# Optimization experiments

Measured on AMD Instinct MI355X. Metric: run time of the kernel, lower is better.

Reference implementation:

```python
import jax, jax.numpy as jnp
import numpy as np

B, K, H, W = 8, 32, 480, 480
N, D = 576, 1024
NUM_CLASSES, CLS_DIM, OUT = 150, 64, 256
IN_DIM = D + CLS_DIM + 5


def setup_inputs() -> dict:
    key = jax.random.key(0)
    ks = jax.random.split(key, 8)
    return {
        "feature_map": jax.random.normal(ks[0], (B, N, D), dtype=jnp.float32),
        "masks": jax.random.randint(ks[1], (B, K, H, W), 0, 2, dtype=jnp.int32),
        "class_ids": jax.random.randint(ks[2], (B, K), 0, NUM_CLASSES, dtype=jnp.int64),
        "embed_table": jax.random.normal(ks[3], (NUM_CLASSES, CLS_DIM), dtype=jnp.float32),
        "W1": jax.random.normal(ks[4], (IN_DIM, OUT), dtype=jnp.float32) * 0.02,
        "b1": jnp.zeros((OUT,), dtype=jnp.float32),
        "ln_g": jnp.ones((OUT,), dtype=jnp.float32),
        "ln_b": jnp.zeros((OUT,), dtype=jnp.float32),
        "W2": jax.random.normal(ks[5], (OUT, OUT), dtype=jnp.float32) * 0.02,
        "b2": jnp.zeros((OUT,), dtype=jnp.float32),
    }


def _geom_feats(m):
    # m: [B,K,H,W] float binary masks -> [B,K,5] (cx, cy, area_norm, bbox_w, bbox_h)
    dt = m.dtype
    area = m.sum((-2, -1))                      # [B,K]
    safe = jnp.maximum(area, 1.0)
    xs = jnp.arange(W, dtype=dt)
    ys = jnp.arange(H, dtype=dt)
    cx = jnp.einsum('bkhw,w->bk', m, xs) / safe / W
    cy = jnp.einsum('bkhw,h->bk', m, ys) / safe / H
    col = m.max(axis=2)                          # [B,K,W] column occupancy
    row = m.max(axis=3)                          # [B,K,H] row occupancy
    x_min = jnp.min(jnp.where(col > 0, xs, float(W)), axis=-1)
    x_max = jnp.max(jnp.where(col > 0, xs, -1.0), axis=-1)
    y_min = jnp.min(jnp.where(row > 0, ys, float(H)), axis=-1)
    y_max = jnp.max(jnp.where(row > 0, ys, -1.0), axis=-1)
    bbox_w = (x_max - x_min + 1.0) / W
    bbox_h = (y_max - y_min + 1.0) / H
    area_norm = area / (H * W)
    geom = jnp.stack([cx, cy, area_norm, bbox_w, bbox_h], axis=-1)  # [B,K,5]
    valid = (area >= 1.0)[..., None]
    return jnp.where(valid, geom, 0.0)


def reference(feature_map, masks, class_ids, embed_table, W1, b1, ln_g, ln_b, W2, b2):
    Hf = Wf = int(round(N ** 0.5))  # 24
    m = (masks > 0).astype(feature_map.dtype)           # [B,K,H,W]
    # nearest-neighbor downsample (PyTorch 'nearest': src = floor(dst*in/out))
    idx_h = (jnp.arange(Hf) * H) // Hf
    idx_w = (jnp.arange(Wf) * W) // Wf
    m_rs = m[:, :, idx_h][:, :, :, idx_w]               # [B,K,Hf,Wf]
    m_flat = m_rs.reshape(B, K, Hf * Wf)                # [B,K,N]
    msum = jnp.clip(m_flat.sum(-1, keepdims=True), 1e-6, None)
    pooled = jnp.einsum('bkn,bnd->bkd', m_flat, feature_map) / msum  # [B,K,D]
    geom = _geom_feats(m)                               # [B,K,5]
    cls_emb = embed_table[class_ids]                    # [B,K,CLS_DIM]
    x = jnp.concatenate([pooled, cls_emb, geom], axis=-1)  # [B,K,IN_DIM]
    h = jax.nn.gelu(x @ W1 + b1, approximate=False)
    mu = h.mean(-1, keepdims=True)
    var = jnp.mean((h - mu) ** 2, axis=-1, keepdims=True)
    hn = (h - mu) * jax.lax.rsqrt(var + 1e-5) * ln_g + ln_b
    return hn @ W2 + b2                                 # [B,K,OUT]
```

## Files before the change

kernel.cpp:

```cpp
#include <hip/hip_runtime.h>
#include <math.h>

#define Bb 8
#define Kk 32
#define Hh 480
#define Ww 480
#define Nn 576
#define Dd 1024
#define CLSD 64
#define OUTD 256
#define INDIM 1093
#define INPAD 1152
#define BK 256
#define PIX4 57600

#define DS_OFF   0
#define META_OFF 147456
#define X_OFF    149504

__global__ __launch_bounds__(1024) void kA(const int* __restrict__ masks,
                                           float* __restrict__ ws) {
  const int bk = blockIdx.x;
  const int t  = threadIdx.x;
  const int4* mp = (const int4*)(masks + (size_t)bk * (Hh * Ww));

  __shared__ float ds[576];
  __shared__ int s_area, s_sumx, s_sumy, s_cnt;
  __shared__ int s_minx, s_maxx, s_miny, s_maxy;
  if (t == 0) {
    s_area = 0; s_sumx = 0; s_sumy = 0; s_cnt = 0;
    s_minx = Ww; s_maxx = -1; s_miny = Hh; s_maxy = -1;
  }
  __syncthreads();

  int area = 0, sumx = 0, sumy = 0, cntds = 0;
  int minx = Ww, maxx = -1, miny = Hh, maxy = -1;

  for (int q = t; q < PIX4; q += 1024) {
    int4 v = mp[q];
    int h   = q / 120;
    int rem = q - h * 120;
    int w0  = rem * 4;
    int m0 = v.x > 0, m1 = v.y > 0, m2 = v.z > 0, m3 = v.w > 0;
    int c = m0 + m1 + m2 + m3;
    area += c;
    sumy += h * c;
    sumx += w0 * c + m1 + 2 * m2 + 3 * m3;
    if (c) {
      miny = min(miny, h);
      maxy = max(maxy, h);
      int lo = m0 ? w0 : (m1 ? w0 + 1 : (m2 ? w0 + 2 : w0 + 3));
      int hi = m3 ? w0 + 3 : (m2 ? w0 + 2 : (m1 ? w0 + 1 : w0));
      minx = min(minx, lo);
      maxx = max(maxx, hi);
    }
    int a20 = h / 20;
    int c5  = rem / 5;
    if (h == a20 * 20 && rem == c5 * 5) {
      ds[a20 * 24 + c5] = (float)m0;
      cntds += m0;
    }
  }

  for (int off = 32; off; off >>= 1) {
    area  += __shfl_down(area, off);
    sumx  += __shfl_down(sumx, off);
    sumy  += __shfl_down(sumy, off);
    cntds += __shfl_down(cntds, off);
    minx = min(minx, __shfl_down(minx, off));
    maxx = max(maxx, __shfl_down(maxx, off));
    miny = min(miny, __shfl_down(miny, off));
    maxy = max(maxy, __shfl_down(maxy, off));
  }
  if ((t & 63) == 0) {
    atomicAdd(&s_area, area);
    atomicAdd(&s_sumx, sumx);
    atomicAdd(&s_sumy, sumy);
    atomicAdd(&s_cnt, cntds);
    atomicMin(&s_minx, minx);
    atomicMax(&s_maxx, maxx);
    atomicMin(&s_miny, miny);
    atomicMax(&s_maxy, maxy);
  }
  __syncthreads();

  float* ws_ds = ws + DS_OFF + (size_t)bk * 576;
  if (t < 576) ws_ds[t] = ds[t];

  if (t == 0) {
    float* meta = ws + META_OFF + (size_t)bk * 8;
    float areaf = (float)s_area;
    float safe  = fmaxf(areaf, 1.0f);
    float cx = ((float)s_sumx / safe) * (1.0f / Ww);
    float cy = ((float)s_sumy / safe) * (1.0f / Hh);
    float an = areaf * (1.0f / (Hh * Ww));
    float bw = (float)(s_maxx - s_minx + 1) * (1.0f / Ww);
    float bh = (float)(s_maxy - s_miny + 1) * (1.0f / Hh);
    if (s_area < 1) { cx = 0.f; cy = 0.f; an = 0.f; bw = 0.f; bh = 0.f; }
    meta[0] = cx; meta[1] = cy; meta[2] = an; meta[3] = bw; meta[4] = bh;
    meta[5] = 1.0f / fmaxf((float)s_cnt, 1e-6f);
    meta[6] = (float)s_cnt;
  }
}

__global__ __launch_bounds__(256) void kB(const float* __restrict__ fm,
                                          const int* __restrict__ cids,
                                          const float* __restrict__ emb,
                                          float* __restrict__ ws) {
  const int b  = blockIdx.x & 7;
  const int k  = blockIdx.x >> 3;
  const int bk = b * Kk + k;
  const int t  = threadIdx.x;

  __shared__ float msh[576];
  __shared__ int act[576];
  __shared__ int nact;
  if (t == 0) nact = 0;
  __syncthreads();

  const float* ws_ds = ws + DS_OFF + (size_t)bk * 576;
  for (int i = t; i < 576; i += 256) {
    float mv = ws_ds[i];
    msh[i] = mv;
    if (mv != 0.0f) {
      int p = atomicAdd(&nact, 1);
      act[p] = i;
    }
  }
  __syncthreads();
  const int na = nact;

  float ax = 0.f, ay = 0.f, az = 0.f, aw = 0.f;
  const float4* fmp = (const float4*)fm + (size_t)b * Nn * (Dd / 4);
  int j = 0;
  for (; j + 4 <= na; j += 4) {
    int4 nn = *(const int4*)(act + j);
    float4 f0 = fmp[nn.x * (Dd / 4) + t];
    float4 f1 = fmp[nn.y * (Dd / 4) + t];
    float4 f2 = fmp[nn.z * (Dd / 4) + t];
    float4 f3 = fmp[nn.w * (Dd / 4) + t];
    ax += f0.x + f1.x + f2.x + f3.x;
    ay += f0.y + f1.y + f2.y + f3.y;
    az += f0.z + f1.z + f2.z + f3.z;
    aw += f0.w + f1.w + f2.w + f3.w;
  }
  for (; j < na; j++) {
    float4 f = fmp[act[j] * (Dd / 4) + t];
    ax += f.x; ay += f.y; az += f.z; aw += f.w;
  }

  const float* meta = ws + META_OFF + (size_t)bk * 8;
  float inv = meta[5];
  float* xrow = ws + X_OFF + (size_t)bk * INPAD;
  float4 p4;
  p4.x = ax * inv; p4.y = ay * inv; p4.z = az * inv; p4.w = aw * inv;
  ((float4*)xrow)[t] = p4;

  if (t < CLSD) {
    int cid = cids[bk];
    xrow[Dd + t] = emb[cid * CLSD + t];
  } else if (t < CLSD + 5) {
    xrow[Dd + CLSD + (t - CLSD)] = meta[t - CLSD];
  } else if (t < CLSD + 5 + (INPAD - INDIM)) {
    xrow[INDIM + (t - CLSD - 5)] = 0.0f;
  }
}

__global__ __launch_bounds__(256) void kC(float* __restrict__ ws,
                                          const float* __restrict__ W1,
                                          const float* __restrict__ b1,
                                          const float* __restrict__ lg,
                                          const float* __restrict__ lb,
                                          const float* __restrict__ W2,
                                          const float* __restrict__ b2,
                                          float* __restrict__ out) {
  const int o  = threadIdx.x;
  const int r0 = blockIdx.x * 2;
  const float* x0 = ws + X_OFF + (size_t)r0 * INPAD;
  const float* x1 = x0 + INPAD;

  float a0 = b1[o], a1 = b1[o];
  for (int i = 0; i < 1092; i += 4) {
    float4 va = *(const float4*)(x0 + i);
    float4 vb = *(const float4*)(x1 + i);
    const float* fa = (const float*)&va;
    const float* fb = (const float*)&vb;
#pragma unroll
    for (int jj = 0; jj < 4; jj++) {
      float w = W1[(i + jj) * OUTD + o];
      a0 = fmaf(fa[jj], w, a0);
      a1 = fmaf(fb[jj], w, a1);
    }
  }
  {
    float w = W1[1092 * OUTD + o];
    a0 = fmaf(x0[1092], w, a0);
    a1 = fmaf(x1[1092], w, a1);
  }

  a0 = 0.5f * a0 * (1.0f + erff(a0 * 0.7071067811865475f));
  a1 = 0.5f * a1 * (1.0f + erff(a1 * 0.7071067811865475f));

  __shared__ float sm0[4], sv0[4], sm1[4], sv1[4];
  float s0 = a0, q0 = a0 * a0, s1 = a1, q1 = a1 * a1;
  for (int off = 32; off; off >>= 1) {
    s0 += __shfl_down(s0, off);
    q0 += __shfl_down(q0, off);
    s1 += __shfl_down(s1, off);
    q1 += __shfl_down(q1, off);
  }
  const int wid = o >> 6, lane = o & 63;
  if (lane == 0) { sm0[wid] = s0; sv0[wid] = q0; sm1[wid] = s1; sv1[wid] = q1; }
  __syncthreads();
  float mu0 = (sm0[0] + sm0[1] + sm0[2] + sm0[3]) * (1.0f / OUTD);
  float mu1 = (sm1[0] + sm1[1] + sm1[2] + sm1[3]) * (1.0f / OUTD);
  float va0 = (sv0[0] + sv0[1] + sv0[2] + sv0[3]) * (1.0f / OUTD) - mu0 * mu0;
  float va1 = (sv1[0] + sv1[1] + sv1[2] + sv1[3]) * (1.0f / OUTD) - mu1 * mu1;
  float is0 = 1.0f / sqrtf(va0 + 1e-5f);
  float is1 = 1.0f / sqrtf(va1 + 1e-5f);
  float g = lg[o], bb = lb[o];
  float h0 = (a0 - mu0) * is0 * g + bb;
  float h1 = (a1 - mu1) * is1 * g + bb;

  float* wsh = ws + DS_OFF;
  wsh[(size_t)r0 * OUTD + o] = h0;
  wsh[(size_t)(r0 + 1) * OUTD + o] = h1;
  __threadfence_block();
  __syncthreads();

  const float* h0p = wsh + (size_t)r0 * OUTD;
  const float* h1p = h0p + OUTD;
  float c0 = b2[o], c1 = b2[o];
  for (int i = 0; i < OUTD; i += 4) {
    float4 ha = *(const float4*)(h0p + i);
    float4 hb = *(const float4*)(h1p + i);
    const float* fa = (const float*)&ha;
    const float* fb = (const float*)&hb;
#pragma unroll
    for (int jj = 0; jj < 4; jj++) {
      float w = W2[(i + jj) * OUTD + o];
      c0 = fmaf(fa[jj], w, c0);
      c1 = fmaf(fb[jj], w, c1);
    }
  }
  out[(size_t)r0 * OUTD + o] = c0;
  out[(size_t)(r0 + 1) * OUTD + o] = c1;
}

extern "C" void kernel_launch(void* const* d_in, const int* in_sizes, int n_in,
                              void* d_out, int out_size, void* d_ws, size_t ws_size,
                              hipStream_t stream) {
  const float* fm    = (const float*)d_in[0];
  const int*   masks = (const int*)d_in[1];
  const int*   cids  = (const int*)d_in[2];
  const float* emb   = (const float*)d_in[3];
  const float* W1    = (const float*)d_in[4];
  const float* b1    = (const float*)d_in[5];
  const float* lg    = (const float*)d_in[6];
  const float* lb    = (const float*)d_in[7];
  const float* W2    = (const float*)d_in[8];
  const float* b2    = (const float*)d_in[9];
  float* out = (float*)d_out;
  float* ws  = (float*)d_ws;

  hipLaunchKernelGGL(kA, dim3(BK), dim3(1024), 0, stream, masks, ws);
  hipLaunchKernelGGL(kB, dim3(BK), dim3(256), 0, stream, fm, cids, emb, ws);
  hipLaunchKernelGGL(kC, dim3(BK / 2), dim3(256), 0, stream, ws, W1, b1, lg, lb, W2, b2, out);
}
```

Measured before the change: 426.9 us.

## Fuse pooling and MLP kernels, split K across waves, unroll mask scan

Merges the pooling kernel and the MLP kernel into one, keeping the input row in shared memory instead of round-tripping through the workspace. The first GEMV now splits the 1093-long input across four waves, with each lane computing four outputs, and reduces the partials in shared memory. Each block handles one row instead of two, which doubles block count but also doubles W1/W2 reads per row. The mask-scan loop in kA gets a fixed trip count with unroll 4 to allow more loads in flight.

```diff
diff --git a/kernel.cpp b/kernel.cpp
--- a/kernel.cpp
+++ b/kernel.cpp
@@ -10,13 +10,11 @@
 #define CLSD 64
 #define OUTD 256
 #define INDIM 1093
-#define INPAD 1152
 #define BK 256
 #define PIX4 57600
 
 #define DS_OFF   0
 #define META_OFF 147456
-#define X_OFF    149504
 
 __global__ __launch_bounds__(1024) void kA(const int* __restrict__ masks,
                                            float* __restrict__ ws) {
@@ -36,8 +34,7 @@
   int area = 0, sumx = 0, sumy = 0, cntds = 0;
   int minx = Ww, maxx = -1, miny = Hh, maxy = -1;
 
-  for (int q = t; q < PIX4; q += 1024) {
-    int4 v = mp[q];
+  auto body = [&](int q, int4 v) {
     int h   = q / 120;
     int rem = q - h * 120;
     int w0  = rem * 4;
@@ -60,6 +57,16 @@
       ds[a20 * 24 + c5] = (float)m0;
       cntds += m0;
     }
+  };
+
+#pragma unroll 4
+  for (int i = 0; i < 56; i++) {
+    int q = t + (i << 10);
+    body(q, mp[q]);
+  }
+  if (t < 256) {
+    int q = 57344 + t;
+    body(q, mp[q]);
   }
 
   for (int off = 32; off; off >>= 1) {
@@ -103,33 +110,46 @@
   }
 }
 
-__global__ __launch_bounds__(256) void kB(const float* __restrict__ fm,
-                                          const int* __restrict__ cids,
-                                          const float* __restrict__ emb,
-                                          float* __restrict__ ws) {
-  const int b  = blockIdx.x & 7;
-  const int k  = blockIdx.x >> 3;
-  const int bk = b * Kk + k;
-  const int t  = threadIdx.x;
-
-  __shared__ float msh[576];
-  __shared__ int act[576];
-  __shared__ int nact;
+__global__ __launch_bounds__(256) void kBC(const float* __restrict__ fm,
+                                           const int* __restrict__ cids,
+                                           const float* __restrict__ emb,
+                                           const float* __restrict__ W1,
+                                           const float* __restrict__ b1,
+                                           const float* __restrict__ lg,
+                                           const float* __restrict__ lb,
+                                           const float* __restrict__ W2,
+                                           const float* __restrict__ b2,
+                                           const float* __restrict__ ws,
+                                           float* __restrict__ out) {
+  const int b    = blockIdx.x & 7;
+  const int k    = blockIdx.x >> 3;
+  const int bk   = b * Kk + k;
+  const int t    = threadIdx.x;
+  const int lane = t & 63;
+  const int w    = t >> 6;
+
+  __shared__ float4 x4s[292];
+  __shared__ int   act[576];
+  __shared__ int   nact;
+  __shared__ float partial[4 * 256];
+  __shared__ float hrow[256];
+  __shared__ float red[8];
+  float* x = (float*)x4s;
+
   if (t == 0) nact = 0;
   __syncthreads();
 
-  const float* ws_ds = ws + DS_OFF + (size_t)bk * 576;
+  const float* dsrow = ws + DS_OFF + (size_t)bk * 576;
   for (int i = t; i < 576; i += 256) {
-    float mv = ws_ds[i];
-    msh[i] = mv;
-    if (mv != 0.0f) {
-      int p = atomicAdd(&nact, 1);
-      act[p] = i;
-    }
-  }
+    float mv = dsrow[i];
+    if (mv != 0.0f) act[atomicAdd(&nact, 1)] = i;
+  }
+  if (t < 75) x[1093 + t] = 0.0f;
   __syncthreads();
   const int na = nact;
 
+  const float* meta = ws + META_OFF + (size_t)bk * 8;
+  float inv = meta[5];
   float ax = 0.f, ay = 0.f, az = 0.f, aw = 0.f;
   const float4* fmp = (const float4*)fm + (size_t)b * Nn * (Dd / 4);
   int j = 0;
@@ -148,103 +168,70 @@
     float4 f = fmp[act[j] * (Dd / 4) + t];
     ax += f.x; ay += f.y; az += f.z; aw += f.w;
   }
-
-  const float* meta = ws + META_OFF + (size_t)bk * 8;
-  float inv = meta[5];
-  float* xrow = ws + X_OFF + (size_t)bk * INPAD;
-  float4 p4;
-  p4.x = ax * inv; p4.y = ay * inv; p4.z = az * inv; p4.w = aw * inv;
-  ((float4*)xrow)[t] = p4;
-
-  if (t < CLSD) {
-    int cid = cids[bk];
-    xrow[Dd + t] = emb[cid * CLSD + t];
-  } else if (t < CLSD + 5) {
-    xrow[Dd + CLSD + (t - CLSD)] = meta[t - CLSD];
-  } else if (t < CLSD + 5 + (INPAD - INDIM)) {
-    xrow[INDIM + (t - CLSD - 5)] = 0.0f;
-  }
-}
-
-__global__ __launch_bounds__(256) void kC(float* __restrict__ ws,
-                                          const float* __restrict__ W1,
-                                          const float* __restrict__ b1,
-                                          const float* __restrict__ lg,
-                                          const float* __restrict__ lb,
-                                          const float* __restrict__ W2,
-                                          const float* __restrict__ b2,
-                                          float* __restrict__ out) {
-  const int o  = threadIdx.x;
-  const int r0 = blockIdx.x * 2;
-  const float* x0 = ws + X_OFF + (size_t)r0 * INPAD;
-  const float* x1 = x0 + INPAD;
-
-  float a0 = b1[o], a1 = b1[o];
-  for (int i = 0; i < 1092; i += 4) {
-    float4 va = *(const float4*)(x0 + i);
-    float4 vb = *(const float4*)(x1 + i);
-    const float* fa = (const float*)&va;
-    const float* fb = (const float*)&vb;
+  float4 p;
+  p.x = ax * inv; p.y = ay * inv; p.z = az * inv; p.w = aw * inv;
+  x4s[t] = p;
+  if (t < CLSD) x[Dd + t] = emb[(size_t)cids[bk] * CLSD + t];
+  else if (t < CLSD + 5) x[Dd + t] = meta[t - CLSD];
+  __syncthreads();
+
+  const int kbeg = w * 292;
+  const int kend = min(INDIM, kbeg + 292);
+  float acc0 = 0.f, acc1 = 0.f, acc2 = 0.f, acc3 = 0.f;
+  int kk = kbeg;
+  for (; kk + 4 <= kend; kk += 4) {
+    float4 xv = x4s[kk >> 2];
+    const float* xs = (const float*)&xv;
 #pragma unroll
-    for (int jj = 0; jj < 4; jj++) {
-      float w = W1[(i + jj) * OUTD + o];
-      a0 = fmaf(fa[jj], w, a0);
-      a1 = fmaf(fb[jj], w, a1);
+    for (int u = 0; u < 4; u++) {
+      float xval = xs[u];
+      const float* wrow = W1 + (size_t)(kk + u) * OUTD;
+      acc0 = fmaf(xval, wrow[lane], acc0);
+      acc1 = fmaf(xval, wrow[lane + 64], acc1);
+      acc2 = fmaf(xval, wrow[lane + 128], acc2);
+      acc3 = fmaf(xval, wrow[lane + 192], acc3);
     }
   }
-  {
-    float w = W1[1092 * OUTD + o];
-    a0 = fmaf(x0[1092], w, a0);
-    a1 = fmaf(x1[1092], w, a1);
-  }
-
-  a0 = 0.5f * a0 * (1.0f + erff(a0 * 0.7071067811865475f));
-  a1 = 0.5f * a1 * (1.0f + erff(a1 * 0.7071067811865475f));
-
-  __shared__ float sm0[4], sv0[4], sm1[4], sv1[4];
-  float s0 = a0, q0 = a0 * a0, s1 = a1, q1 = a1 * a1;
+  for (; kk < kend; kk++) {
+    float xval = x[kk];
+    const float* wrow = W1 + (size_t)kk * OUTD;
+    acc0 = fmaf(xval, wrow[lane], acc0);
+    acc1 = fmaf(xval, wrow[lane + 64], acc1);
+    acc2 = fmaf(xval, wrow[lane + 128], acc2);
+    acc3 = fmaf(xval, wrow[lane + 192], acc3);
+  }
+  partial[w * 256 + lane] = acc0;
+  partial[w * 256 + lane + 64] = acc1;
+  partial[w * 256 + lane + 128] = acc2;
+  partial[w * 256 + lane + 192] = acc3;
+  __syncthreads();
+
+  float hval = partial[t] + partial[256 + t] + partial[512 + t] + partial[768 + t] + b1[t];
+  hval = 0.5f * hval * (1.0f + erff(hval * 0.7071067811865475f));
+  float s = hval, q = hval * hval;
   for (int off = 32; off; off >>= 1) {
-    s0 += __shfl_down(s0, off);
-    q0 += __shfl_down(q0, off);
-    s1 += __shfl_down(s1, off);
-    q1 += __shfl_down(q1, off);
-  }
-  const int wid = o >> 6, lane = o & 63;
-  if (lane == 0) { sm0[wid] = s0; sv0[wid] = q0; sm1[wid] = s1; sv1[wid] = q1; }
-  __syncthreads();
-  float mu0 = (sm0[0] + sm0[1] + sm0[2] + sm0[3]) * (1.0f / OUTD);
-  float mu1 = (sm1[0] + sm1[1] + sm1[2] + sm1[3]) * (1.0f / OUTD);
-  float va0 = (sv0[0] + sv0[1] + sv0[2] + sv0[3]) * (1.0f / OUTD) - mu0 * mu0;
-  float va1 = (sv1[0] + sv1[1] + sv1[2] + sv1[3]) * (1.0f / OUTD) - mu1 * mu1;
-  float is0 = 1.0f / sqrtf(va0 + 1e-5f);
-  float is1 = 1.0f / sqrtf(va1 + 1e-5f);
-  float g = lg[o], bb = lb[o];
-  float h0 = (a0 - mu0) * is0 * g + bb;
-  float h1 = (a1 - mu1) * is1 * g + bb;
-
-  float* wsh = ws + DS_OFF;
-  wsh[(size_t)r0 * OUTD + o] = h0;
-  wsh[(size_t)(r0 + 1) * OUTD + o] = h1;
-  __threadfence_block();
-  __syncthreads();
-
-  const float* h0p = wsh + (size_t)r0 * OUTD;
-  const float* h1p = h0p + OUTD;
-  float c0 = b2[o], c1 = b2[o];
-  for (int i = 0; i < OUTD; i += 4) {
-    float4 ha = *(const float4*)(h0p + i);
-    float4 hb = *(const float4*)(h1p + i);
-    const float* fa = (const float*)&ha;
-    const float* fb = (const float*)&hb;
+    s += __shfl_down(s, off);
+    q += __shfl_down(q, off);
+  }
+  if (lane == 0) { red[w] = s; red[4 + w] = q; }
+  __syncthreads();
+  float mu  = (red[0] + red[1] + red[2] + red[3]) * (1.0f / OUTD);
+  float var = (red[4] + red[5] + red[6] + red[7]) * (1.0f / OUTD) - mu * mu;
+  float ist = 1.0f / sqrtf(var + 1e-5f);
+  float hn  = (hval - mu) * ist * lg[t] + lb[t];
+  hrow[t] = hn;
+  __syncthreads();
+
+  float c = b2[t];
+  const float4* h4 = (const float4*)hrow;
+  for (int i = 0; i < 64; i++) {
+    float4 hv = h4[i];
+    const float* hs = (const float*)&hv;
 #pragma unroll
-    for (int jj = 0; jj < 4; jj++) {
-      float w = W2[(i + jj) * OUTD + o];
-      c0 = fmaf(fa[jj], w, c0);
-      c1 = fmaf(fb[jj], w, c1);
-    }
-  }
-  out[(size_t)r0 * OUTD + o] = c0;
-  out[(size_t)(r0 + 1) * OUTD + o] = c1;
+    for (int u = 0; u < 4; u++)
+      c = fmaf(hs[u], W2[(size_t)(i * 4 + u) * OUTD + t], c);
+  }
+  out[(size_t)bk * OUTD + t] = c;
 }
 
 extern "C" void kernel_launch(void* const* d_in, const int* in_sizes, int n_in,
@@ -264,6 +251,6 @@
   float* ws  = (float*)d_ws;
 
   hipLaunchKernelGGL(kA, dim3(BK), dim3(1024), 0, stream, masks, ws);
-  hipLaunchKernelGGL(kB, dim3(BK), dim3(256), 0, stream, fm, cids, emb, ws);
-  hipLaunchKernelGGL(kC, dim3(BK / 2), dim3(256), 0, stream, ws, W1, b1, lg, lb, W2, b2, out);
+  hipLaunchKernelGGL(kBC, dim3(BK), dim3(256), 0, stream, fm, cids, emb,
+                     W1, b1, lg, lb, W2, b2, ws, out);
 }
```

Measured after the change: 415.4 us. -2.7%, faster.
